# Optimization experiments

Hardware: AMD Instinct MI355X
Metric: run time of the kernel (lower is better)

The kernel has to match this reference:

```python
import math
import jax
import jax.numpy as jnp
import numpy as np
from jax import lax

NH = 256       # n_hidden
KS = 5         # kernel_size
STRIDE = 2
DEPTH_VARIANT = True
B = 64
T = 4096


def _conv1d(x, w, b, stride):
    # x: [B, Cin, L], w: [Cout, Cin, K], torch-style symmetric padding (K-1)//2
    p = (w.shape[2] - 1) // 2
    y = lax.conv_general_dilated(x, w, window_strides=(stride,),
                                 padding=[(p, p)],
                                 dimension_numbers=('NCH', 'OIH', 'NCH'))
    return y + b[None, :, None]


def _seq_mask(x, N):
    m = jnp.arange(x.shape[2])[None, :] < N[:, None]
    return x * m[:, None, :].astype(x.dtype)


def setup_inputs() -> dict:
    key = jax.random.key(0)
    k1, k2, k3, k4, k5, k6 = jax.random.split(key, 6)
    h = jax.random.normal(k1, (B, NH, T), dtype=jnp.float32)
    N = jax.random.randint(k2, (B,), 1, T + 1, dtype=jnp.int32)
    cin1 = NH + (1 if DEPTH_VARIANT else 0)
    s1 = 1.0 / math.sqrt(cin1 * KS)
    s2 = 1.0 / math.sqrt(NH * KS)
    w1 = jax.random.uniform(k3, (2 * NH, cin1, KS), jnp.float32, -s1, s1)
    b1 = jax.random.uniform(k4, (2 * NH,), jnp.float32, -s1, s1)
    w2 = jax.random.uniform(k5, (NH, NH, KS), jnp.float32, -s2, s2)
    b2 = jax.random.uniform(k6, (NH,), jnp.float32, -s2, s2)
    return {"h": h, "N": N, "w1": w1, "b1": b1, "w2": w2, "b2": b2}


def reference(h, N, w1, b1, w2, b2):
    # Faithful to torch Reduce.forward (eval mode, dropout=0).
    # Instead of dynamically pruning finished rows, run all rows for the full
    # (statically known) number of reductions and capture h[:, :, 0] at the
    # depth where each row's N first drops to <= 1. The original output order
    # (grouped by finishing depth, original order within a group) is recovered
    # by a stable argsort on finish depth.
    nh = NH
    batch = h.shape[0]
    captured = jnp.zeros((batch, nh), h.dtype)
    finish_depth = jnp.zeros((batch,), jnp.int32)
    done = jnp.zeros((batch,), bool)
    depth = 0
    while True:
        if DEPTH_VARIANT:
            d = jnp.full((batch, 1, h.shape[2]), math.log1p(depth), h.dtype)
            hh = jnp.concatenate([h, d], axis=1)
        else:
            hh = h
        hh = _seq_mask(hh, N)
        lr = _conv1d(hh, w1, b1, STRIDE)
        N = (N - 1) // STRIDE + 1  # floor((N-1)/stride) + 1
        l = lr[:, :nh]
        r = jax.nn.relu(lr[:, nh:])
        r = _seq_mask(r, N)
        r = _conv1d(r, w2, b2, 1)
        h = jax.nn.relu(l + r)
        newly = (~done) & (N <= 1)
        captured = jnp.where(newly[:, None], h[:, :, 0], captured)
        finish_depth = jnp.where(newly, depth, finish_depth)
        done = done | newly
        depth += 1
        if h.shape[2] <= 1:  # static time length; N <= L so all rows are done
            break
    order = jnp.argsort(finish_depth, stable=True)
    return captured[order]
```

## Files before the change

kernel.cpp:

```cpp
#include <hip/hip_runtime.h>
#include <cmath>
#include <cstdint>


typedef __attribute__((ext_vector_type(8))) __bf16 bf16x8;
typedef __attribute__((ext_vector_type(4))) float f32x4;

union U16B { uint4 u; bf16x8 b; };
__device__ __forceinline__ bf16x8 as_bf16x8(uint4 u) { U16B x; x.u = u; return x.b; }

__device__ __forceinline__ unsigned short bf_hi_bits(float x) {
    union { __bf16 b; unsigned short s; } u; u.b = (__bf16)x; return u.s;
}
__device__ __forceinline__ float bf_hi_f(float x) { return (float)(__bf16)x; }

#define MFMA(a, b, c) __builtin_amdgcn_mfma_f32_16x16x32_bf16(a, b, c, 0, 0, 0)

__global__ void setup_kernel(const int* __restrict__ N0, int* __restrict__ rankfd) {
    __shared__ int fd_s[64];
    int b = threadIdx.x;
    int n = N0[b];
    int d = 0;
    while ((1 << (d + 1)) < n) ++d;
    fd_s[b] = d;
    __syncthreads();
    int myfd = fd_s[b];
    int r = 0;
    for (int i = 0; i < 64; ++i) {
        int f = fd_s[i];
        r += (f < myfd || (f == myfd && i < b)) ? 1 : 0;
    }
    rankfd[b] = r;
    rankfd[64 + b] = myfd;
}

__global__ void prepack_kernel(const float* __restrict__ w1, const float* __restrict__ w2,
                               unsigned short* __restrict__ Whi1, unsigned short* __restrict__ Wlo1,
                               unsigned short* __restrict__ Whi2, unsigned short* __restrict__ Wlo2,
                               float* __restrict__ wd1, float* __restrict__ wsum1) {
    const int T1 = 40 * 32 * 512;
    const int T2 = 40 * 16 * 512;
    int id = blockIdx.x * 256 + threadIdx.x;
    if (id < T1) {
        int chunk = id >> 14;
        int rem = id & 16383;
        int ot = rem >> 9;
        int rem2 = rem & 511;
        int l = rem2 >> 3, j = rem2 & 7;
        int k = chunk >> 3, cc = chunk & 7;
        int oc = ot * 16 + (l & 15);
        int c = cc * 32 + (l >> 4) * 8 + j;
        float wv = w1[oc * 1285 + c * 5 + k];
        Whi1[id] = bf_hi_bits(wv);
        Wlo1[id] = bf_hi_bits(wv - bf_hi_f(wv));
    } else if (id < T1 + T2) {
        int base = id - T1;
        int chunk = base >> 13;
        int rem = base & 8191;
        int ot = rem >> 9;
        int rem2 = rem & 511;
        int l = rem2 >> 3, j = rem2 & 7;
        int k = chunk >> 3, cc = chunk & 7;
        int oc = ot * 16 + (l & 15);
        int c = cc * 32 + (l >> 4) * 8 + j;
        float wv = w2[oc * 1280 + c * 5 + k];
        Whi2[base] = bf_hi_bits(wv);
        Wlo2[base] = bf_hi_bits(wv - bf_hi_f(wv));
    } else if (id < T1 + T2 + 512) {
        int oc = id - T1 - T2;
        float s = 0.f;
        for (int k = 0; k < 5; ++k) {
            float wv = w1[oc * 1285 + 1280 + k];
            wd1[oc * 5 + k] = wv;
            s += wv;
        }
        wsum1[oc] = s;
    }
}

__global__ __launch_bounds__(256, 4)
void transpose_kernel(const float* __restrict__ h, const int* __restrict__ N0,
                      char* __restrict__ H) {
    __shared__ unsigned short sm[2 * 64 * 140];
    const int tid = threadIdx.x;
    const int b = blockIdx.z;
    const int c0 = blockIdx.y * 64;
    const int t0 = blockIdx.x * 128;
    const int n0 = N0[b];
    const int lane32 = tid & 31;
    for (int it = 0; it < 8; ++it) {
        int cl = (tid >> 5) * 8 + it;
        const float* src = h + ((size_t)(b * 256 + c0 + cl)) * 4096 + t0 + lane32 * 4;
        float4 v = *(const float4*)src;
        int gt = t0 + lane32 * 4;
        float f[4] = {v.x, v.y, v.z, v.w};
        ushort4 hi, lo;
        unsigned short* hp = &hi.x;
        unsigned short* lp = &lo.x;
#pragma unroll
        for (int e = 0; e < 4; ++e) {
            float x = (gt + e < n0) ? f[e] : 0.f;
            float xh = bf_hi_f(x);
            hp[e] = bf_hi_bits(x);
            lp[e] = bf_hi_bits(x - xh);
        }
        *(ushort4*)(&sm[cl * 140 + lane32 * 4]) = hi;
        *(ushort4*)(&sm[8960 + cl * 140 + lane32 * 4]) = lo;
    }
    __syncthreads();
    const int sub = tid & 7;
    const int rowp = tid >> 3;
    for (int rep = 0; rep < 8; ++rep) {
        int idx = rowp + 32 * rep;
        int tl = idx >> 1;
        int plane = idx & 1;
        union { unsigned short s[8]; uint4 u; } pk;
#pragma unroll
        for (int j = 0; j < 8; ++j)
            pk.s[j] = sm[plane * 8960 + (sub * 8 + j) * 140 + tl];
        char* dst = H + ((size_t)(b * 4096) + t0 + tl) * 1024 + plane * 512 + c0 * 2 + sub * 16;
        *(uint4*)dst = pk.u;
    }
}

__global__ __launch_bounds__(256, 4)
void conv1_kernel(const char* __restrict__ Hin,
                  const unsigned short* __restrict__ Whi, const unsigned short* __restrict__ Wlo,
                  const float* __restrict__ b1, const float* __restrict__ wd1,
                  const float* __restrict__ wsum1, const int* __restrict__ N0,
                  float* __restrict__ Lout, char* __restrict__ Rout,
                  int T_in, int T_out, int depth, float logd) {
    __shared__ __align__(16) char smem[132 * 256];
    const int tid = threadIdx.x;
    const int w = tid >> 6, l = tid & 63;
    const int b = blockIdx.z;
    const int t0 = blockIdx.x * 64;
    const int n0 = N0[b];
    const int Nb = (n0 + (1 << depth) - 1) >> depth;
    const int Nn = (Nb + 1) >> 1;

    if (t0 >= Nn) {
        if (blockIdx.y == 1) {
            int row = t0 + (tid >> 2);
            if (row < T_out) {
                char* rp = Rout + ((size_t)(b * T_out) + row) * 1024 + (tid & 3) * 256;
                uint4 z = make_uint4(0, 0, 0, 0);
#pragma unroll
                for (int qq = 0; qq < 16; ++qq) *(uint4*)(rp + qq * 16) = z;
            }
        }
        return;
    }

    f32x4 acc[4][4];
#pragma unroll
    for (int i = 0; i < 4; ++i)
#pragma unroll
        for (int j = 0; j < 4; ++j) acc[i][j] = f32x4{0.f, 0.f, 0.f, 0.f};

    const int base_p = 2 * t0 - 2;
    const int otg_base = blockIdx.y * 16 + w * 4;

    const int sg_g8 = l & 7;
    const int sg_seg = (l >> 3) & 1;
    const int sg_rb0 = tid >> 4;

#pragma unroll 1
    for (int q0 = 0; q0 < 4; ++q0) {
        if (q0) __syncthreads();
        for (int rb = sg_rb0; rb < 132; rb += 16) {
            int p = base_p + rb;
            uint4 v = make_uint4(0, 0, 0, 0);
            if (p >= 0 && p < T_in)
                v = *(const uint4*)(Hin + ((size_t)(b * T_in) + p) * 1024 + sg_seg * 512 + q0 * 128 + sg_g8 * 16);
            int s = (rb >> 1) + (rb & 1) * 66;
            int phys = (sg_g8 ^ (s & 7)) | (sg_seg << 3);
            *(uint4*)(smem + s * 256 + phys * 16) = v;
        }
        __syncthreads();
#pragma unroll
        for (int k = 0; k < 5; ++k) {
#pragma unroll
            for (int ccl = 0; ccl < 2; ++ccl) {
                const int chunk = k * 8 + q0 * 2 + ccl;
                bf16x8 Bh[4], Bl[4];
#pragma unroll
                for (int tt = 0; tt < 4; ++tt) {
                    int s = tt * 16 + (l & 15) + (k >> 1) + (k & 1) * 66;
                    int gB = ccl * 4 + (l >> 4);
                    int ph = gB ^ (s & 7);
                    Bh[tt] = as_bf16x8(*(const uint4*)(smem + s * 256 + ph * 16));
                    Bl[tt] = as_bf16x8(*(const uint4*)(smem + s * 256 + (ph | 8) * 16));
                }
#pragma unroll
                for (int ot = 0; ot < 4; ++ot) {
                    size_t aoff = ((size_t)(chunk * 32 + otg_base + ot)) * 512 + l * 8;
                    bf16x8 Ah = as_bf16x8(*(const uint4*)(Whi + aoff));
                    bf16x8 Al = as_bf16x8(*(const uint4*)(Wlo + aoff));
#pragma unroll
                    for (int tt = 0; tt < 4; ++tt) {
                        acc[ot][tt] = MFMA(Ah, Bh[tt], acc[ot][tt]);
                        acc[ot][tt] = MFMA(Ah, Bl[tt], acc[ot][tt]);
                        acc[ot][tt] = MFMA(Al, Bh[tt], acc[ot][tt]);
                    }
                }
            }
        }
    }

    const int q = l >> 4;
    const int n = l & 15;
    const bool is_r = (blockIdx.y == 1);
#pragma unroll
    for (int ot = 0; ot < 4; ++ot) {
        const int ocg0 = (otg_base + ot) * 16 + q * 4;
        float4 bias = *(const float4*)(b1 + ocg0);
        float4 ws4 = *(const float4*)(wsum1 + ocg0);
#pragma unroll
        for (int tt = 0; tt < 4; ++tt) {
            int t = t0 + tt * 16 + n;
            if (t >= T_out) continue;
            float v0 = acc[ot][tt].x, v1 = acc[ot][tt].y, v2 = acc[ot][tt].z, v3 = acc[ot][tt].w;
            if (depth > 0) {
                if (t >= 1 && 2 * t + 2 < Nb) {
                    v0 += logd * ws4.x; v1 += logd * ws4.y;
                    v2 += logd * ws4.z; v3 += logd * ws4.w;
                } else {
                    float ind[5];
#pragma unroll
                    for (int k = 0; k < 5; ++k) {
                        int p = 2 * t + k - 2;
                        ind[k] = (p >= 0 && p < Nb) ? logd : 0.f;
                    }
                    float sv[4] = {0.f, 0.f, 0.f, 0.f};
#pragma unroll
                    for (int j = 0; j < 4; ++j)
#pragma unroll
                        for (int k = 0; k < 5; ++k) sv[j] += ind[k] * wd1[(ocg0 + j) * 5 + k];
                    v0 += sv[0]; v1 += sv[1]; v2 += sv[2]; v3 += sv[3];
                }
            }
            v0 += bias.x; v1 += bias.y; v2 += bias.z; v3 += bias.w;
            if (!is_r) {
                float4 o; o.x = v0; o.y = v1; o.z = v2; o.w = v3;
                *(float4*)(Lout + ((size_t)(b * T_out) + t) * 256 + ocg0) = o;
            } else {
                bool live = (t < Nn);
                float r0v = live ? fmaxf(v0, 0.f) : 0.f;
                float r1v = live ? fmaxf(v1, 0.f) : 0.f;
                float r2v = live ? fmaxf(v2, 0.f) : 0.f;
                float r3v = live ? fmaxf(v3, 0.f) : 0.f;
                int ocr = ocg0 - 256;
                char* rrow = Rout + ((size_t)(b * T_out) + t) * 1024;
                ushort4 H, L2;
                H.x = bf_hi_bits(r0v); L2.x = bf_hi_bits(r0v - bf_hi_f(r0v));
                H.y = bf_hi_bits(r1v); L2.y = bf_hi_bits(r1v - bf_hi_f(r1v));
                H.z = bf_hi_bits(r2v); L2.z = bf_hi_bits(r2v - bf_hi_f(r2v));
                H.w = bf_hi_bits(r3v); L2.w = bf_hi_bits(r3v - bf_hi_f(r3v));
                *(ushort4*)(rrow + ocr * 2) = H;
                *(ushort4*)(rrow + 512 + ocr * 2) = L2;
            }
        }
    }
}

__global__ __launch_bounds__(256, 4)
void conv2_kernel(const char* __restrict__ Rin,
                  const unsigned short* __restrict__ Whi, const unsigned short* __restrict__ Wlo,
                  const float* __restrict__ b2, const int* __restrict__ N0,
                  const int* __restrict__ rankfd, float* __restrict__ LH,
                  float* __restrict__ out, int T, int depth) {
    __shared__ __align__(16) char smem[68 * 512];
    const int tid = threadIdx.x;
    const int w = tid >> 6, l = tid & 63;
    const int b = blockIdx.z;
    const int t0 = blockIdx.x * 64;
    const int n0 = N0[b];
    const int Nn = (n0 + (1 << (depth + 1)) - 1) >> (depth + 1);

    if (t0 >= Nn) {
        int row = t0 + (tid >> 2);
        if (row < T) {
            char* hp = (char*)LH + ((size_t)(b * T) + row) * 1024 + (tid & 3) * 256;
            uint4 z = make_uint4(0, 0, 0, 0);
#pragma unroll
            for (int qq = 0; qq < 16; ++qq) *(uint4*)(hp + qq * 16) = z;
        }
        return;
    }

    f32x4 acc[4][4];
#pragma unroll
    for (int i = 0; i < 4; ++i)
#pragma unroll
        for (int j = 0; j < 4; ++j) acc[i][j] = f32x4{0.f, 0.f, 0.f, 0.f};

    const int sg_g16 = l & 15;
    const int sg_seg = (l >> 4) & 1;
    const int sg_rb0 = w * 2 + (l >> 5);

#pragma unroll 1
    for (int hf = 0; hf < 2; ++hf) {
        if (hf) __syncthreads();
        for (int rb = sg_rb0; rb < 68; rb += 8) {
            int p = t0 - 2 + rb;
            uint4 v = make_uint4(0, 0, 0, 0);
            if (p >= 0 && p < T)
                v = *(const uint4*)(Rin + ((size_t)(b * T) + p) * 1024 + sg_seg * 512 + hf * 256 + sg_g16 * 16);
            int phys = (sg_g16 ^ (rb & 7)) | (sg_seg << 4);
            *(uint4*)(smem + rb * 512 + phys * 16) = v;
        }
        __syncthreads();
#pragma unroll
        for (int k = 0; k < 5; ++k) {
#pragma unroll
            for (int cc = 0; cc < 4; ++cc) {
                const int chunk = k * 8 + hf * 4 + cc;
                bf16x8 Bh[4], Bl[4];
#pragma unroll
                for (int tt = 0; tt < 4; ++tt) {
                    int s = tt * 16 + (l & 15) + k;
                    int gq = cc * 4 + (l >> 4);
                    int ph = gq ^ (s & 7);
                    Bh[tt] = as_bf16x8(*(const uint4*)(smem + s * 512 + ph * 16));
                    Bl[tt] = as_bf16x8(*(const uint4*)(smem + s * 512 + (ph | 16) * 16));
                }
#pragma unroll
                for (int ot = 0; ot < 4; ++ot) {
                    size_t aoff = ((size_t)(chunk * 16 + w * 4 + ot)) * 512 + l * 8;
                    bf16x8 Ah = as_bf16x8(*(const uint4*)(Whi + aoff));
                    bf16x8 Al = as_bf16x8(*(const uint4*)(Wlo + aoff));
#pragma unroll
                    for (int tt = 0; tt < 4; ++tt) {
                        acc[ot][tt] = MFMA(Ah, Bh[tt], acc[ot][tt]);
                        acc[ot][tt] = MFMA(Ah, Bl[tt], acc[ot][tt]);
                        acc[ot][tt] = MFMA(Al, Bh[tt], acc[ot][tt]);
                    }
                }
            }
        }
    }

    const int q = l >> 4;
    const int n = l & 15;
    const int rk = rankfd[b];
    const int fd = rankfd[64 + b];
#pragma unroll
    for (int ot = 0; ot < 4; ++ot) {
        const int ocg0 = (w * 4 + ot) * 16 + q * 4;
        float4 bias = *(const float4*)(b2 + ocg0);
#pragma unroll
        for (int tt = 0; tt < 4; ++tt) {
            int t = t0 + tt * 16 + n;
            float v0 = 0.f, v1 = 0.f, v2 = 0.f, v3 = 0.f;
            if (t < T && t < Nn) {
                float4 l4 = *(const float4*)(LH + ((size_t)(b * T) + t) * 256 + ocg0);
                v0 = fmaxf(acc[ot][tt].x + l4.x + bias.x, 0.f);
                v1 = fmaxf(acc[ot][tt].y + l4.y + bias.y, 0.f);
                v2 = fmaxf(acc[ot][tt].z + l4.z + bias.z, 0.f);
                v3 = fmaxf(acc[ot][tt].w + l4.w + bias.w, 0.f);
                if (t == 0 && depth == fd) {
                    float4 o; o.x = v0; o.y = v1; o.z = v2; o.w = v3;
                    *(float4*)(out + rk * 256 + ocg0) = o;
                }
            }
            acc[ot][tt] = f32x4{v0, v1, v2, v3};
        }
    }
    __syncthreads();
#pragma unroll
    for (int ot = 0; ot < 4; ++ot) {
        const int ocg0 = (w * 4 + ot) * 16 + q * 4;
#pragma unroll
        for (int tt = 0; tt < 4; ++tt) {
            int t = t0 + tt * 16 + n;
            if (t >= T) continue;
            char* hrow = (char*)LH + ((size_t)(b * T) + t) * 1024;
            float v0 = acc[ot][tt].x, v1 = acc[ot][tt].y, v2 = acc[ot][tt].z, v3 = acc[ot][tt].w;
            ushort4 H, L2;
            H.x = bf_hi_bits(v0); L2.x = bf_hi_bits(v0 - bf_hi_f(v0));
            H.y = bf_hi_bits(v1); L2.y = bf_hi_bits(v1 - bf_hi_f(v1));
            H.z = bf_hi_bits(v2); L2.z = bf_hi_bits(v2 - bf_hi_f(v2));
            H.w = bf_hi_bits(v3); L2.w = bf_hi_bits(v3 - bf_hi_f(v3));
            *(ushort4*)(hrow + ocg0 * 2) = H;
            *(ushort4*)(hrow + 512 + ocg0 * 2) = L2;
        }
    }
}

extern "C" void kernel_launch(void* const* d_in, const int* in_sizes, int n_in,
                              void* d_out, int out_size, void* d_ws, size_t ws_size,
                              hipStream_t stream) {
    const float* h  = (const float*)d_in[0];
    const int*   N0 = (const int*)d_in[1];
    const float* w1 = (const float*)d_in[2];
    const float* b1 = (const float*)d_in[3];
    const float* w2 = (const float*)d_in[4];
    const float* b2 = (const float*)d_in[5];
    float* out = (float*)d_out;

    char* ws = (char*)d_ws;
    size_t off = 0;
    auto alloc = [&](size_t bytes) -> void* {
        void* p = ws + off;
        off = (off + bytes + 255) & ~(size_t)255;
        return p;
    };
    int* rankfd            = (int*)alloc(512);
    float* wd1             = (float*)alloc(512 * 5 * 4);
    float* wsum1           = (float*)alloc(512 * 4);
    unsigned short* Whi1   = (unsigned short*)alloc((size_t)655360 * 2);
    unsigned short* Wlo1   = (unsigned short*)alloc((size_t)655360 * 2);
    unsigned short* Whi2   = (unsigned short*)alloc((size_t)327680 * 2);
    unsigned short* Wlo2   = (unsigned short*)alloc((size_t)327680 * 2);
    float* P1              = (float*)alloc((size_t)64 * 2048 * 1024);
    char*  H4096           = (char*)alloc((size_t)64 * 4096 * 1024);
    float* P0              = (float*)H4096;
    char*  R               = (char*)alloc((size_t)64 * 2048 * 1024);
    (void)ws_size;

    setup_kernel<<<1, 64, 0, stream>>>(N0, rankfd);
    {
        int total = 655360 + 327680 + 512;
        prepack_kernel<<<(total + 255) / 256, 256, 0, stream>>>(w1, w2, Whi1, Wlo1, Whi2, Wlo2, wd1, wsum1);
    }
    transpose_kernel<<<dim3(32, 4, 64), 256, 0, stream>>>(h, N0, H4096);

    int T_in = 4096;
    for (int d = 0; d < 12; ++d) {
        int To = T_in >> 1;
        float* LH = (d & 1) ? P0 : P1;
        const char* Hin = (d == 0) ? (const char*)H4096 : (const char*)((d & 1) ? P1 : P0);
        float logd = log1pf((float)d);
        dim3 g1((To + 63) / 64, 2, 64);
        conv1_kernel<<<g1, 256, 0, stream>>>(Hin, Whi1, Wlo1, b1, wd1, wsum1, N0,
                                             LH, R, T_in, To, d, logd);
        dim3 g2((To + 63) / 64, 1, 64);
        conv2_kernel<<<g2, 256, 0, stream>>>(R, Whi2, Wlo2, b2, N0, rankfd, LH, out, To, d);
        T_in = To;
    }
}
```

Measured before the change: 2.842 ms.

## Use persistent blocks with atomic work-queue scheduling for conv kernels

Replaces the 3D grid launch of both conv kernels with a persistent-block grid capped at 1024 blocks that pull work items from a global atomic counter, one counter per kernel per depth, zeroed in the setup kernel. Items are ordered batch-fastest, so early time tiles across all batches are claimed first and short, early-exiting tiles (rows past N) are spread dynamically. The goal is better load balance and less block launch overhead when many tiles are skipped or zero-filled. It adds an atomic plus two barriers per item and may reduce occupancy-driven latency hiding.

```diff
diff --git a/kernel.cpp b/kernel.cpp
--- a/kernel.cpp
+++ b/kernel.cpp
@@ -16,9 +16,11 @@
 
 #define MFMA(a, b, c) __builtin_amdgcn_mfma_f32_16x16x32_bf16(a, b, c, 0, 0, 0)
 
-__global__ void setup_kernel(const int* __restrict__ N0, int* __restrict__ rankfd) {
+__global__ void setup_kernel(const int* __restrict__ N0, int* __restrict__ rankfd,
+                             int* __restrict__ ctrs) {
     __shared__ int fd_s[64];
     int b = threadIdx.x;
+    if (b < 32) ctrs[b] = 0;
     int n = N0[b];
     int d = 0;
     while ((1 << (d + 1)) < n) ++d;
@@ -129,136 +131,147 @@
                   const float* __restrict__ b1, const float* __restrict__ wd1,
                   const float* __restrict__ wsum1, const int* __restrict__ N0,
                   float* __restrict__ Lout, char* __restrict__ Rout,
-                  int T_in, int T_out, int depth, float logd) {
+                  int T_in, int T_out, int depth, float logd,
+                  int* __restrict__ ctr, int NI) {
     __shared__ __align__(16) char smem[132 * 256];
+    __shared__ int s_it;
     const int tid = threadIdx.x;
     const int w = tid >> 6, l = tid & 63;
-    const int b = blockIdx.z;
-    const int t0 = blockIdx.x * 64;
-    const int n0 = N0[b];
-    const int Nb = (n0 + (1 << depth) - 1) >> depth;
-    const int Nn = (Nb + 1) >> 1;
-
-    if (t0 >= Nn) {
-        if (blockIdx.y == 1) {
-            int row = t0 + (tid >> 2);
-            if (row < T_out) {
-                char* rp = Rout + ((size_t)(b * T_out) + row) * 1024 + (tid & 3) * 256;
-                uint4 z = make_uint4(0, 0, 0, 0);
-#pragma unroll
-                for (int qq = 0; qq < 16; ++qq) *(uint4*)(rp + qq * 16) = z;
-            }
-        }
-        return;
-    }
-
-    f32x4 acc[4][4];
-#pragma unroll
-    for (int i = 0; i < 4; ++i)
-#pragma unroll
-        for (int j = 0; j < 4; ++j) acc[i][j] = f32x4{0.f, 0.f, 0.f, 0.f};
-
-    const int base_p = 2 * t0 - 2;
-    const int otg_base = blockIdx.y * 16 + w * 4;
-
     const int sg_g8 = l & 7;
     const int sg_seg = (l >> 3) & 1;
     const int sg_rb0 = tid >> 4;
 
+    for (;;) {
+        if (tid == 0) s_it = atomicAdd(ctr, 1);
+        __syncthreads();
+        const int item = s_it;
+        __syncthreads();
+        if (item >= NI) break;
+
+        const int b = item & 63;
+        const int y = (item >> 6) & 1;
+        const int t0 = (item >> 7) * 64;
+        const int n0 = N0[b];
+        const int Nb = (n0 + (1 << depth) - 1) >> depth;
+        const int Nn = (Nb + 1) >> 1;
+
+        if (t0 >= Nn) {
+            if (y == 1) {
+                int row = t0 + (tid >> 2);
+                if (row < T_out) {
+                    char* rp = Rout + ((size_t)(b * T_out) + row) * 1024 + (tid & 3) * 256;
+                    uint4 z = make_uint4(0, 0, 0, 0);
+#pragma unroll
+                    for (int qq = 0; qq < 16; ++qq) *(uint4*)(rp + qq * 16) = z;
+                }
+            }
+            continue;
+        }
+
+        f32x4 acc[4][4];
+#pragma unroll
+        for (int i = 0; i < 4; ++i)
+#pragma unroll
+            for (int j = 0; j < 4; ++j) acc[i][j] = f32x4{0.f, 0.f, 0.f, 0.f};
+
+        const int base_p = 2 * t0 - 2;
+        const int otg_base = y * 16 + w * 4;
+
 #pragma unroll 1
-    for (int q0 = 0; q0 < 4; ++q0) {
-        if (q0) __syncthreads();
-        for (int rb = sg_rb0; rb < 132; rb += 16) {
-            int p = base_p + rb;
-            uint4 v = make_uint4(0, 0, 0, 0);
-            if (p >= 0 && p < T_in)
-                v = *(const uint4*)(Hin + ((size_t)(b * T_in) + p) * 1024 + sg_seg * 512 + q0 * 128 + sg_g8 * 16);
-            int s = (rb >> 1) + (rb & 1) * 66;
-            int phys = (sg_g8 ^ (s & 7)) | (sg_seg << 3);
-            *(uint4*)(smem + s * 256 + phys * 16) = v;
-        }
-        __syncthreads();
-#pragma unroll
-        for (int k = 0; k < 5; ++k) {
-#pragma unroll
-            for (int ccl = 0; ccl < 2; ++ccl) {
-                const int chunk = k * 8 + q0 * 2 + ccl;
-                bf16x8 Bh[4], Bl[4];
-#pragma unroll
-                for (int tt = 0; tt < 4; ++tt) {
-                    int s = tt * 16 + (l & 15) + (k >> 1) + (k & 1) * 66;
-                    int gB = ccl * 4 + (l >> 4);
-                    int ph = gB ^ (s & 7);
-                    Bh[tt] = as_bf16x8(*(const uint4*)(smem + s * 256 + ph * 16));
-                    Bl[tt] = as_bf16x8(*(const uint4*)(smem + s * 256 + (ph | 8) * 16));
-                }
-#pragma unroll
-                for (int ot = 0; ot < 4; ++ot) {
-                    size_t aoff = ((size_t)(chunk * 32 + otg_base + ot)) * 512 + l * 8;
-                    bf16x8 Ah = as_bf16x8(*(const uint4*)(Whi + aoff));
-                    bf16x8 Al = as_bf16x8(*(const uint4*)(Wlo + aoff));
+        for (int q0 = 0; q0 < 4; ++q0) {
+            if (q0) __syncthreads();
+            for (int rb = sg_rb0; rb < 132; rb += 16) {
+                int p = base_p + rb;
+                uint4 v = make_uint4(0, 0, 0, 0);
+                if (p >= 0 && p < T_in)
+                    v = *(const uint4*)(Hin + ((size_t)(b * T_in) + p) * 1024 + sg_seg * 512 + q0 * 128 + sg_g8 * 16);
+                int s = (rb >> 1) + (rb & 1) * 66;
+                int phys = (sg_g8 ^ (s & 7)) | (sg_seg << 3);
+                *(uint4*)(smem + s * 256 + phys * 16) = v;
+            }
+            __syncthreads();
+#pragma unroll
+            for (int k = 0; k < 5; ++k) {
+#pragma unroll
+                for (int ccl = 0; ccl < 2; ++ccl) {
+                    const int chunk = k * 8 + q0 * 2 + ccl;
+                    bf16x8 Bh[4], Bl[4];
 #pragma unroll
                     for (int tt = 0; tt < 4; ++tt) {
-                        acc[ot][tt] = MFMA(Ah, Bh[tt], acc[ot][tt]);
-                        acc[ot][tt] = MFMA(Ah, Bl[tt], acc[ot][tt]);
-                        acc[ot][tt] = MFMA(Al, Bh[tt], acc[ot][tt]);
-                    }
-                }
-            }
-        }
-    }
-
-    const int q = l >> 4;
-    const int n = l & 15;
-    const bool is_r = (blockIdx.y == 1);
-#pragma unroll
-    for (int ot = 0; ot < 4; ++ot) {
-        const int ocg0 = (otg_base + ot) * 16 + q * 4;
-        float4 bias = *(const float4*)(b1 + ocg0);
-        float4 ws4 = *(const float4*)(wsum1 + ocg0);
-#pragma unroll
-        for (int tt = 0; tt < 4; ++tt) {
-            int t = t0 + tt * 16 + n;
-            if (t >= T_out) continue;
-            float v0 = acc[ot][tt].x, v1 = acc[ot][tt].y, v2 = acc[ot][tt].z, v3 = acc[ot][tt].w;
-            if (depth > 0) {
-                if (t >= 1 && 2 * t + 2 < Nb) {
-                    v0 += logd * ws4.x; v1 += logd * ws4.y;
-                    v2 += logd * ws4.z; v3 += logd * ws4.w;
+                        int s = tt * 16 + (l & 15) + (k >> 1) + (k & 1) * 66;
+                        int gB = ccl * 4 + (l >> 4);
+                        int ph = gB ^ (s & 7);
+                        Bh[tt] = as_bf16x8(*(const uint4*)(smem + s * 256 + ph * 16));
+                        Bl[tt] = as_bf16x8(*(const uint4*)(smem + s * 256 + (ph | 8) * 16));
+                    }
+#pragma unroll
+                    for (int ot = 0; ot < 4; ++ot) {
+                        size_t aoff = ((size_t)(chunk * 32 + otg_base + ot)) * 512 + l * 8;
+                        bf16x8 Ah = as_bf16x8(*(const uint4*)(Whi + aoff));
+                        bf16x8 Al = as_bf16x8(*(const uint4*)(Wlo + aoff));
+#pragma unroll
+                        for (int tt = 0; tt < 4; ++tt) {
+                            acc[ot][tt] = MFMA(Ah, Bh[tt], acc[ot][tt]);
+                            acc[ot][tt] = MFMA(Ah, Bl[tt], acc[ot][tt]);
+                            acc[ot][tt] = MFMA(Al, Bh[tt], acc[ot][tt]);
+                        }
+                    }
+                }
+            }
+        }
+
+        const int q = l >> 4;
+        const int n = l & 15;
+        const bool is_r = (y == 1);
+#pragma unroll
+        for (int ot = 0; ot < 4; ++ot) {
+            const int ocg0 = (otg_base + ot) * 16 + q * 4;
+            float4 bias = *(const float4*)(b1 + ocg0);
+            float4 ws4 = *(const float4*)(wsum1 + ocg0);
+#pragma unroll
+            for (int tt = 0; tt < 4; ++tt) {
+                int t = t0 + tt * 16 + n;
+                if (t >= T_out) continue;
+                float v0 = acc[ot][tt].x, v1 = acc[ot][tt].y, v2 = acc[ot][tt].z, v3 = acc[ot][tt].w;
+                if (depth > 0) {
+                    if (t >= 1 && 2 * t + 2 < Nb) {
+                        v0 += logd * ws4.x; v1 += logd * ws4.y;
+                        v2 += logd * ws4.z; v3 += logd * ws4.w;
+                    } else {
+                        float ind[5];
+#pragma unroll
+                        for (int k = 0; k < 5; ++k) {
+                            int p = 2 * t + k - 2;
+                            ind[k] = (p >= 0 && p < Nb) ? logd : 0.f;
+                        }
+                        float sv[4] = {0.f, 0.f, 0.f, 0.f};
+#pragma unroll
+                        for (int j = 0; j < 4; ++j)
+#pragma unroll
+                            for (int k = 0; k < 5; ++k) sv[j] += ind[k] * wd1[(ocg0 + j) * 5 + k];
+                        v0 += sv[0]; v1 += sv[1]; v2 += sv[2]; v3 += sv[3];
+                    }
+                }
+                v0 += bias.x; v1 += bias.y; v2 += bias.z; v3 += bias.w;
+                if (!is_r) {
+                    float4 o; o.x = v0; o.y = v1; o.z = v2; o.w = v3;
+                    *(float4*)(Lout + ((size_t)(b * T_out) + t) * 256 + ocg0) = o;
                 } else {
-                    float ind[5];
-#pragma unroll
-                    for (int k = 0; k < 5; ++k) {
-                        int p = 2 * t + k - 2;
-                        ind[k] = (p >= 0 && p < Nb) ? logd : 0.f;
-                    }
-                    float sv[4] = {0.f, 0.f, 0.f, 0.f};
-#pragma unroll
-                    for (int j = 0; j < 4; ++j)
-#pragma unroll
-                        for (int k = 0; k < 5; ++k) sv[j] += ind[k] * wd1[(ocg0 + j) * 5 + k];
-                    v0 += sv[0]; v1 += sv[1]; v2 += sv[2]; v3 += sv[3];
-                }
-            }
-            v0 += bias.x; v1 += bias.y; v2 += bias.z; v3 += bias.w;
-            if (!is_r) {
-                float4 o; o.x = v0; o.y = v1; o.z = v2; o.w = v3;
-                *(float4*)(Lout + ((size_t)(b * T_out) + t) * 256 + ocg0) = o;
-            } else {
-                bool live = (t < Nn);
-                float r0v = live ? fmaxf(v0, 0.f) : 0.f;
-                float r1v = live ? fmaxf(v1, 0.f) : 0.f;
-                float r2v = live ? fmaxf(v2, 0.f) : 0.f;
-                float r3v = live ? fmaxf(v3, 0.f) : 0.f;
-                int ocr = ocg0 - 256;
-                char* rrow = Rout + ((size_t)(b * T_out) + t) * 1024;
-                ushort4 H, L2;
-                H.x = bf_hi_bits(r0v); L2.x = bf_hi_bits(r0v - bf_hi_f(r0v));
-                H.y = bf_hi_bits(r1v); L2.y = bf_hi_bits(r1v - bf_hi_f(r1v));
-                H.z = bf_hi_bits(r2v); L2.z = bf_hi_bits(r2v - bf_hi_f(r2v));
-                H.w = bf_hi_bits(r3v); L2.w = bf_hi_bits(r3v - bf_hi_f(r3v));
-                *(ushort4*)(rrow + ocr * 2) = H;
-                *(ushort4*)(rrow + 512 + ocr * 2) = L2;
+                    bool live = (t < Nn);
+                    float r0v = live ? fmaxf(v0, 0.f) : 0.f;
+                    float r1v = live ? fmaxf(v1, 0.f) : 0.f;
+                    float r2v = live ? fmaxf(v2, 0.f) : 0.f;
+                    float r3v = live ? fmaxf(v3, 0.f) : 0.f;
+                    int ocr = ocg0 - 256;
+                    char* rrow = Rout + ((size_t)(b * T_out) + t) * 1024;
+                    ushort4 H, L2;
+                    H.x = bf_hi_bits(r0v); L2.x = bf_hi_bits(r0v - bf_hi_f(r0v));
+                    H.y = bf_hi_bits(r1v); L2.y = bf_hi_bits(r1v - bf_hi_f(r1v));
+                    H.z = bf_hi_bits(r2v); L2.z = bf_hi_bits(r2v - bf_hi_f(r2v));
+                    H.w = bf_hi_bits(r3v); L2.w = bf_hi_bits(r3v - bf_hi_f(r3v));
+                    *(ushort4*)(rrow + ocr * 2) = H;
+                    *(ushort4*)(rrow + 512 + ocr * 2) = L2;
+                }
             }
         }
     }
@@ -269,121 +282,131 @@
                   const unsigned short* __restrict__ Whi, const unsigned short* __restrict__ Wlo,
                   const float* __restrict__ b2, const int* __restrict__ N0,
                   const int* __restrict__ rankfd, float* __restrict__ LH,
-                  float* __restrict__ out, int T, int depth) {
+                  float* __restrict__ out, int T, int depth,
+                  int* __restrict__ ctr, int NI) {
     __shared__ __align__(16) char smem[68 * 512];
+    __shared__ int s_it;
     const int tid = threadIdx.x;
     const int w = tid >> 6, l = tid & 63;
-    const int b = blockIdx.z;
-    const int t0 = blockIdx.x * 64;
-    const int n0 = N0[b];
-    const int Nn = (n0 + (1 << (depth + 1)) - 1) >> (depth + 1);
-
-    if (t0 >= Nn) {
-        int row = t0 + (tid >> 2);
-        if (row < T) {
-            char* hp = (char*)LH + ((size_t)(b * T) + row) * 1024 + (tid & 3) * 256;
-            uint4 z = make_uint4(0, 0, 0, 0);
-#pragma unroll
-            for (int qq = 0; qq < 16; ++qq) *(uint4*)(hp + qq * 16) = z;
-        }
-        return;
-    }
-
-    f32x4 acc[4][4];
-#pragma unroll
-    for (int i = 0; i < 4; ++i)
-#pragma unroll
-        for (int j = 0; j < 4; ++j) acc[i][j] = f32x4{0.f, 0.f, 0.f, 0.f};
-
     const int sg_g16 = l & 15;
     const int sg_seg = (l >> 4) & 1;
     const int sg_rb0 = w * 2 + (l >> 5);
 
+    for (;;) {
+        if (tid == 0) s_it = atomicAdd(ctr, 1);
+        __syncthreads();
+        const int item = s_it;
+        __syncthreads();
+        if (item >= NI) break;
+
+        const int b = item & 63;
+        const int t0 = (item >> 6) * 64;
+        const int n0 = N0[b];
+        const int Nn = (n0 + (1 << (depth + 1)) - 1) >> (depth + 1);
+
+        if (t0 >= Nn) {
+            int row = t0 + (tid >> 2);
+            if (row < T) {
+                char* hp = (char*)LH + ((size_t)(b * T) + row) * 1024 + (tid & 3) * 256;
+                uint4 z = make_uint4(0, 0, 0, 0);
+#pragma unroll
+                for (int qq = 0; qq < 16; ++qq) *(uint4*)(hp + qq * 16) = z;
+            }
+            continue;
+        }
+
+        f32x4 acc[4][4];
+#pragma unroll
+        for (int i = 0; i < 4; ++i)
+#pragma unroll
+            for (int j = 0; j < 4; ++j) acc[i][j] = f32x4{0.f, 0.f, 0.f, 0.f};
+
 #pragma unroll 1
-    for (int hf = 0; hf < 2; ++hf) {
-        if (hf) __syncthreads();
-        for (int rb = sg_rb0; rb < 68; rb += 8) {
-            int p = t0 - 2 + rb;
-            uint4 v = make_uint4(0, 0, 0, 0);
-            if (p >= 0 && p < T)
-                v = *(const uint4*)(Rin + ((size_t)(b * T) + p) * 1024 + sg_seg * 512 + hf * 256 + sg_g16 * 16);
-            int phys = (sg_g16 ^ (rb & 7)) | (sg_seg << 4);
-            *(uint4*)(smem + rb * 512 + phys * 16) = v;
+        for (int hf = 0; hf < 2; ++hf) {
+            if (hf) __syncthreads();
+            for (int rb = sg_rb0; rb < 68; rb += 8) {
+                int p = t0 - 2 + rb;
+                uint4 v = make_uint4(0, 0, 0, 0);
+                if (p >= 0 && p < T)
+                    v = *(const uint4*)(Rin + ((size_t)(b * T) + p) * 1024 + sg_seg * 512 + hf * 256 + sg_g16 * 16);
+                int phys = (sg_g16 ^ (rb & 7)) | (sg_seg << 4);
+                *(uint4*)(smem + rb * 512 + phys * 16) = v;
+            }
+            __syncthreads();
+#pragma unroll
+            for (int k = 0; k < 5; ++k) {
+#pragma unroll
+                for (int cc = 0; cc < 4; ++cc) {
+                    const int chunk = k * 8 + hf * 4 + cc;
+                    bf16x8 Bh[4], Bl[4];
+#pragma unroll
+                    for (int tt = 0; tt < 4; ++tt) {
+                        int s = tt * 16 + (l & 15) + k;
+                        int gq = cc * 4 + (l >> 4);
+                        int ph = gq ^ (s & 7);
+                        Bh[tt] = as_bf16x8(*(const uint4*)(smem + s * 512 + ph * 16));
+                        Bl[tt] = as_bf16x8(*(const uint4*)(smem + s * 512 + (ph | 16) * 16));
+                    }
+#pragma unroll
+                    for (int ot = 0; ot < 4; ++ot) {
+                        size_t aoff = ((size_t)(chunk * 16 + w * 4 + ot)) * 512 + l * 8;
+                        bf16x8 Ah = as_bf16x8(*(const uint4*)(Whi + aoff));
+                        bf16x8 Al = as_bf16x8(*(const uint4*)(Wlo + aoff));
+#pragma unroll
+                        for (int tt = 0; tt < 4; ++tt) {
+                            acc[ot][tt] = MFMA(Ah, Bh[tt], acc[ot][tt]);
+                            acc[ot][tt] = MFMA(Ah, Bl[tt], acc[ot][tt]);
+                            acc[ot][tt] = MFMA(Al, Bh[tt], acc[ot][tt]);
+                        }
+                    }
+                }
+            }
+        }
+
+        const int q = l >> 4;
+        const int n = l & 15;
+        const int rk = rankfd[b];
+        const int fd = rankfd[64 + b];
+#pragma unroll
+        for (int ot = 0; ot < 4; ++ot) {
+            const int ocg0 = (w * 4 + ot) * 16 + q * 4;
+            float4 bias = *(const float4*)(b2 + ocg0);
+#pragma unroll
+            for (int tt = 0; tt < 4; ++tt) {
+                int t = t0 + tt * 16 + n;
+                float v0 = 0.f, v1 = 0.f, v2 = 0.f, v3 = 0.f;
+                if (t < T && t < Nn) {
+                    float4 l4 = *(const float4*)(LH + ((size_t)(b * T) + t) * 256 + ocg0);
+                    v0 = fmaxf(acc[ot][tt].x + l4.x + bias.x, 0.f);
+                    v1 = fmaxf(acc[ot][tt].y + l4.y + bias.y, 0.f);
+                    v2 = fmaxf(acc[ot][tt].z + l4.z + bias.z, 0.f);
+                    v3 = fmaxf(acc[ot][tt].w + l4.w + bias.w, 0.f);
+                    if (t == 0 && depth == fd) {
+                        float4 o; o.x = v0; o.y = v1; o.z = v2; o.w = v3;
+                        *(float4*)(out + rk * 256 + ocg0) = o;
+                    }
+                }
+                acc[ot][tt] = f32x4{v0, v1, v2, v3};
+            }
         }
         __syncthreads();
 #pragma unroll
-        for (int k = 0; k < 5; ++k) {
-#pragma unroll
-            for (int cc = 0; cc < 4; ++cc) {
-                const int chunk = k * 8 + hf * 4 + cc;
-                bf16x8 Bh[4], Bl[4];
-#pragma unroll
-                for (int tt = 0; tt < 4; ++tt) {
-                    int s = tt * 16 + (l & 15) + k;
-                    int gq = cc * 4 + (l >> 4);
-                    int ph = gq ^ (s & 7);
-                    Bh[tt] = as_bf16x8(*(const uint4*)(smem + s * 512 + ph * 16));
-                    Bl[tt] = as_bf16x8(*(const uint4*)(smem + s * 512 + (ph | 16) * 16));
-                }
-#pragma unroll
-                for (int ot = 0; ot < 4; ++ot) {
-                    size_t aoff = ((size_t)(chunk * 16 + w * 4 + ot)) * 512 + l * 8;
-                    bf16x8 Ah = as_bf16x8(*(const uint4*)(Whi + aoff));
-                    bf16x8 Al = as_bf16x8(*(const uint4*)(Wlo + aoff));
-#pragma unroll
-                    for (int tt = 0; tt < 4; ++tt) {
-                        acc[ot][tt] = MFMA(Ah, Bh[tt], acc[ot][tt]);
-                        acc[ot][tt] = MFMA(Ah, Bl[tt], acc[ot][tt]);
-                        acc[ot][tt] = MFMA(Al, Bh[tt], acc[ot][tt]);
-                    }
-                }
-            }
-        }
-    }
-
-    const int q = l >> 4;
-    const int n = l & 15;
-    const int rk = rankfd[b];
-    const int fd = rankfd[64 + b];
-#pragma unroll
-    for (int ot = 0; ot < 4; ++ot) {
-        const int ocg0 = (w * 4 + ot) * 16 + q * 4;
-        float4 bias = *(const float4*)(b2 + ocg0);
-#pragma unroll
-        for (int tt = 0; tt < 4; ++tt) {
-            int t = t0 + tt * 16 + n;
-            float v0 = 0.f, v1 = 0.f, v2 = 0.f, v3 = 0.f;
-            if (t < T && t < Nn) {
-                float4 l4 = *(const float4*)(LH + ((size_t)(b * T) + t) * 256 + ocg0);
-                v0 = fmaxf(acc[ot][tt].x + l4.x + bias.x, 0.f);
-                v1 = fmaxf(acc[ot][tt].y + l4.y + bias.y, 0.f);
-                v2 = fmaxf(acc[ot][tt].z + l4.z + bias.z, 0.f);
-                v3 = fmaxf(acc[ot][tt].w + l4.w + bias.w, 0.f);
-                if (t == 0 && depth == fd) {
-                    float4 o; o.x = v0; o.y = v1; o.z = v2; o.w = v3;
-                    *(float4*)(out + rk * 256 + ocg0) = o;
-                }
-            }
-            acc[ot][tt] = f32x4{v0, v1, v2, v3};
-        }
-    }
-    __syncthreads();
-#pragma unroll
-    for (int ot = 0; ot < 4; ++ot) {
-        const int ocg0 = (w * 4 + ot) * 16 + q * 4;
-#pragma unroll
-        for (int tt = 0; tt < 4; ++tt) {
-            int t = t0 + tt * 16 + n;
-            if (t >= T) continue;
-            char* hrow = (char*)LH + ((size_t)(b * T) + t) * 1024;
-            float v0 = acc[ot][tt].x, v1 = acc[ot][tt].y, v2 = acc[ot][tt].z, v3 = acc[ot][tt].w;
-            ushort4 H, L2;
-            H.x = bf_hi_bits(v0); L2.x = bf_hi_bits(v0 - bf_hi_f(v0));
-            H.y = bf_hi_bits(v1); L2.y = bf_hi_bits(v1 - bf_hi_f(v1));
-            H.z = bf_hi_bits(v2); L2.z = bf_hi_bits(v2 - bf_hi_f(v2));
-            H.w = bf_hi_bits(v3); L2.w = bf_hi_bits(v3 - bf_hi_f(v3));
-            *(ushort4*)(hrow + ocg0 * 2) = H;
-            *(ushort4*)(hrow + 512 + ocg0 * 2) = L2;
+        for (int ot = 0; ot < 4; ++ot) {
+            const int ocg0 = (w * 4 + ot) * 16 + q * 4;
+#pragma unroll
+            for (int tt = 0; tt < 4; ++tt) {
+                int t = t0 + tt * 16 + n;
+                if (t >= T) continue;
+                char* hrow = (char*)LH + ((size_t)(b * T) + t) * 1024;
+                float v0 = acc[ot][tt].x, v1 = acc[ot][tt].y, v2 = acc[ot][tt].z, v3 = acc[ot][tt].w;
+                ushort4 H, L2;
+                H.x = bf_hi_bits(v0); L2.x = bf_hi_bits(v0 - bf_hi_f(v0));
+                H.y = bf_hi_bits(v1); L2.y = bf_hi_bits(v1 - bf_hi_f(v1));
+                H.z = bf_hi_bits(v2); L2.z = bf_hi_bits(v2 - bf_hi_f(v2));
+                H.w = bf_hi_bits(v3); L2.w = bf_hi_bits(v3 - bf_hi_f(v3));
+                *(ushort4*)(hrow + ocg0 * 2) = H;
+                *(ushort4*)(hrow + 512 + ocg0 * 2) = L2;
+            }
         }
     }
 }
@@ -417,9 +440,10 @@
     char*  H4096           = (char*)alloc((size_t)64 * 4096 * 1024);
     float* P0              = (float*)H4096;
     char*  R               = (char*)alloc((size_t)64 * 2048 * 1024);
+    int* ctrs              = (int*)alloc(32 * sizeof(int));
     (void)ws_size;
 
-    setup_kernel<<<1, 64, 0, stream>>>(N0, rankfd);
+    setup_kernel<<<1, 64, 0, stream>>>(N0, rankfd, ctrs);
     {
         int total = 655360 + 327680 + 512;
         prepack_kernel<<<(total + 255) / 256, 256, 0, stream>>>(w1, w2, Whi1, Wlo1, Whi2, Wlo2, wd1, wsum1);
@@ -432,11 +456,16 @@
         float* LH = (d & 1) ? P0 : P1;
         const char* Hin = (d == 0) ? (const char*)H4096 : (const char*)((d & 1) ? P1 : P0);
         float logd = log1pf((float)d);
-        dim3 g1((To + 63) / 64, 2, 64);
+        int gx = (To + 63) / 64;
+        int NI1 = gx * 128;
+        int NI2 = gx * 64;
+        int g1 = NI1 < 1024 ? NI1 : 1024;
+        int g2 = NI2 < 1024 ? NI2 : 1024;
         conv1_kernel<<<g1, 256, 0, stream>>>(Hin, Whi1, Wlo1, b1, wd1, wsum1, N0,
-                                             LH, R, T_in, To, d, logd);
-        dim3 g2((To + 63) / 64, 1, 64);
-        conv2_kernel<<<g2, 256, 0, stream>>>(R, Whi2, Wlo2, b2, N0, rankfd, LH, out, To, d);
+                                             LH, R, T_in, To, d, logd,
+                                             ctrs + 2 * d, NI1);
+        conv2_kernel<<<g2, 256, 0, stream>>>(R, Whi2, Wlo2, b2, N0, rankfd, LH, out, To, d,
+                                             ctrs + 2 * d + 1, NI2);
         T_in = To;
     }
 }
```

New measurement: 3.214 ms. +13.1%, slower.
